# Kernel optimization log

Hardware: AMD Instinct MI355X
Metric: run time of the kernel (lower is better)

The kernel has to match this reference:

```python
import jax, jax.numpy as jnp
import numpy as np
import math

T, S, B, E, H = 2048, 2048, 4, 1024, 16
D = E // H


def setup_inputs() -> dict:
    key = jax.random.key(0)
    ks = jax.random.split(key, 12)
    inp = {
        "query": jax.random.normal(ks[0], (T, B, E), jnp.float32),
        "key": jax.random.normal(ks[1], (S, B, E), jnp.float32),
        "value": jax.random.normal(ks[2], (S, B, E), jnp.float32),
        # causal mask: True means masked (matches torch masked_fill semantics)
        "attn_mask": jnp.triu(jnp.ones((T, S), dtype=bool), k=1),
        # torch Linear layout: weight [out_features, in_features]
        "Wq": jax.random.normal(ks[3], (E, E), jnp.float32) * (1.0 / math.sqrt(E)),
        "bq": jax.random.normal(ks[4], (E,), jnp.float32) * 0.02,
        "Wk": jax.random.normal(ks[5], (E, E), jnp.float32) * (1.0 / math.sqrt(E)),
        "bk": jax.random.normal(ks[6], (E,), jnp.float32) * 0.02,
        "Wv": jax.random.normal(ks[7], (E, E), jnp.float32) * (1.0 / math.sqrt(E)),
        "bv": jax.random.normal(ks[8], (E,), jnp.float32) * 0.02,
        "Wo": jax.random.normal(ks[9], (E, E), jnp.float32) * (1.0 / math.sqrt(E)),
        "bo": jax.random.normal(ks[10], (E,), jnp.float32) * 0.02,
    }
    return inp


def reference(query, key, value, attn_mask, Wq, bq, Wk, bk, Wv, bv, Wo, bo):
    # inputs are [T/S, B, E] (batch_first=False); compute in [B, H, T, D]
    q = (jnp.einsum('tbe,fe->btf', query, Wq) + bq).reshape(B, T, H, D).transpose(0, 2, 1, 3)
    k = (jnp.einsum('sbe,fe->bsf', key, Wk) + bk).reshape(B, S, H, D).transpose(0, 2, 1, 3)
    v = (jnp.einsum('sbe,fe->bsf', value, Wv) + bv).reshape(B, S, H, D).transpose(0, 2, 1, 3)

    scores = jnp.einsum('bhtd,bhsd->bhts', q, k) / math.sqrt(D)  # [B,H,T,S]
    masked = jnp.where(attn_mask[None, None, :, :], -jnp.inf, scores)
    # custom numerics: epsilon-shifted softmax, then re-zero -inf positions
    probs = jax.nn.softmax(masked + 1e-9, axis=-1)
    probs = jnp.where(jnp.isinf(masked), 0.0, probs)

    out = jnp.einsum('bhts,bhsd->bhtd', probs, v)  # [B,H,T,D]
    out = out.transpose(0, 2, 1, 3).reshape(B, T, E)
    out = out @ Wo.T + bo
    return out.transpose(1, 0, 2)  # back to [T, B, E]
```

## Files before the change

### kernel.cpp

```cpp
#include <hip/hip_runtime.h>

typedef unsigned short u16;
typedef __attribute__((ext_vector_type(8))) __bf16 bf16x8;
typedef __attribute__((ext_vector_type(4))) float f32x4;
typedef __attribute__((ext_vector_type(16))) float f32x16;
typedef __attribute__((ext_vector_type(4))) unsigned short u16x4;
typedef __attribute__((ext_vector_type(8))) unsigned short u16x8;
typedef __attribute__((ext_vector_type(4))) unsigned int u32x4;

#define T_LEN 2048
#define B_SZ 4
#define E_DIM 1024
#define H_N 16
#define D_H 64
#define M_ROWS (T_LEN * B_SZ)
#define NQT (T_LEN / 128)

__device__ __forceinline__ u16 f2bf(float f){
  unsigned u = __builtin_bit_cast(unsigned, f);
  u += 0x7fffu + ((u >> 16) & 1u);
  return (u16)(u >> 16);
}

__device__ __forceinline__ float fexp2(float x){
#if __has_builtin(__builtin_amdgcn_exp2f)
  return __builtin_amdgcn_exp2f(x);
#else
  return exp2f(x);
#endif
}

__device__ __forceinline__ unsigned cvtpk(float lo, float hi){
  unsigned w;
  asm("v_cvt_pk_bf16_f32 %0, %1, %2" : "=v"(w) : "v"(lo), "v"(hi));
  return w;
}
__device__ __forceinline__ float xhalf_max(float x){
  return fmaxf(x, __shfl_xor(x, 32));
}
__device__ __forceinline__ float xhalf_sum(float x){
  return x + __shfl_xor(x, 32);
}

__device__ __forceinline__ void load_lds16(const void* g, void* l){
  __builtin_amdgcn_global_load_lds(
      (const __attribute__((address_space(1))) void*)g,
      (__attribute__((address_space(3))) void*)l, 16, 0, 0);
}

__global__ void cvt_all(
    const float* __restrict__ i0, const float* __restrict__ i1, const float* __restrict__ i2,
    const float* __restrict__ i3, const float* __restrict__ i4, const float* __restrict__ i5,
    const float* __restrict__ i6,
    u16* __restrict__ o0, u16* __restrict__ o1, u16* __restrict__ o2,
    u16* __restrict__ o3, u16* __restrict__ o4, u16* __restrict__ o5,
    u16* __restrict__ o6, int nX, int nW)
{
  const int z = blockIdx.z;
  const float* in; u16* out; int n;
  switch (z){
    case 0: in=i0; out=o0; n=nX; break;
    case 1: in=i1; out=o1; n=nX; break;
    case 2: in=i2; out=o2; n=nX; break;
    case 3: in=i3; out=o3; n=nW; break;
    case 4: in=i4; out=o4; n=nW; break;
    case 5: in=i5; out=o5; n=nW; break;
    default: in=i6; out=o6; n=nW; break;
  }
  int idx = (blockIdx.x * blockDim.x + threadIdx.x) * 4;
  int stride = gridDim.x * blockDim.x * 4;
  for (int i = idx; i < n; i += stride){
    float4 v = *(const float4*)(in + i);
    u16x4 o = { f2bf(v.x), f2bf(v.y), f2bf(v.z), f2bf(v.w) };
    *(u16x4*)(out + i) = o;
  }
}

__device__ __forceinline__ void gemm_mainloop(
    const u16* __restrict__ A, const u16* __restrict__ Bt,
    int m0, int n0, u16* As, u16* Bs, f32x4 (&acc)[4][4])
{
  constexpr int K = E_DIM;
  constexpr int NT = K / 32;
  const int tid = threadIdx.x;
  const int lane = tid & 63;
  const int w = tid >> 6;
  const int wr = w >> 1, wc = w & 1;
  const int lr = lane & 15, lg = lane >> 4;

  #pragma unroll
  for (int i=0;i<4;i++)
    #pragma unroll
    for (int j=0;j<4;j++) acc[i][j] = (f32x4){0.f,0.f,0.f,0.f};

  auto STAGE = [&](int t, int b){
    int k0 = t * 32;
    #pragma unroll
    for (int r=0;r<2;++r){
      int c = r*256 + tid;
      int row = c >> 2, cc = (c & 3) * 8;
      load_lds16(A  + (size_t)(m0 + row)*K + k0 + cc,
                 (char*)As + b*8192 + (r*256 + w*64)*16);
      load_lds16(Bt + (size_t)(n0 + row)*K + k0 + cc,
                 (char*)Bs + b*8192 + (r*256 + w*64)*16);
    }
  };

  STAGE(0, 0);
  __syncthreads();
  for (int t = 0; t < NT; ++t){
    const int cur = t & 1;
    if (t + 1 < NT) STAGE(t+1, cur^1);
    bf16x8 af[4], bfr[4];
    #pragma unroll
    for (int i=0;i<4;i++){
      af[i]  = *(const bf16x8*)&As[cur*4096 + (wr*64 + i*16 + lr)*32 + lg*8];
      bfr[i] = *(const bf16x8*)&Bs[cur*4096 + (wc*64 + i*16 + lr)*32 + lg*8];
    }
    #pragma unroll
    for (int i=0;i<4;i++)
      #pragma unroll
      for (int j=0;j<4;j++)
        acc[i][j] = __builtin_amdgcn_mfma_f32_16x16x32_bf16(af[i], bfr[j], acc[i][j], 0,0,0);
    __syncthreads();
  }
}

struct QKVArgs {
  const u16* A[3]; const u16* Bw[3]; const float* bias[3];
  float scale[3]; u16* out[3];
};

__global__ __launch_bounds__(256) void gemm_qkv(QKVArgs args){
  __shared__ __align__(16) u16 As[2*128*32];
  __shared__ __align__(16) u16 Bs[2*128*32];
  const int z = blockIdx.z;
  const int m0 = blockIdx.y * 128, n0 = blockIdx.x * 128;
  f32x4 acc[4][4];
  gemm_mainloop(args.A[z], args.Bw[z], m0, n0, As, Bs, acc);

  const int tid = threadIdx.x;
  const int lane = tid & 63;
  const int w = tid >> 6;
  const int wr = w >> 1, wc = w & 1;
  const int lr = lane & 15, lg = lane >> 4;
  const float* bias = args.bias[z];
  const float scale = args.scale[z];
  u16* outB = args.out[z];
  #pragma unroll
  for (int i=0;i<4;i++)
    #pragma unroll
    for (int j=0;j<4;j++)
      #pragma unroll
      for (int q=0;q<4;q++){
        int m = m0 + wr*64 + i*16 + lg*4 + q;
        int n = n0 + wc*64 + j*16 + lr;
        float v = (acc[i][j][q] + bias[n]) * scale;
        int t = m >> 2, b = m & 3;
        int h = n >> 6, d = n & 63;
        outB[ ((size_t)(b*H_N + h)*T_LEN + t)*D_H + d ] = f2bf(v);
      }
}

__global__ __launch_bounds__(256) void gemm_out(
    const u16* __restrict__ A, const u16* __restrict__ Bt,
    const float* __restrict__ bias, float* __restrict__ outF)
{
  __shared__ __align__(16) u16 As[2*128*32];
  __shared__ __align__(16) u16 Bs[2*128*32];
  const int m0 = blockIdx.y * 128, n0 = blockIdx.x * 128;
  f32x4 acc[4][4];
  gemm_mainloop(A, Bt, m0, n0, As, Bs, acc);

  const int tid = threadIdx.x;
  const int lane = tid & 63;
  const int w = tid >> 6;
  const int wr = w >> 1, wc = w & 1;
  const int lr = lane & 15, lg = lane >> 4;
  #pragma unroll
  for (int i=0;i<4;i++)
    #pragma unroll
    for (int j=0;j<4;j++)
      #pragma unroll
      for (int q=0;q<4;q++){
        int m = m0 + wr*64 + i*16 + lg*4 + q;
        int n = n0 + wc*64 + j*16 + lr;
        float v = acc[i][j][q] + bias[n];
        int b = m >> 11, t = m & 2047;
        outF[ (size_t)(t*B_SZ + b)*E_DIM + n ] = v;
      }
}

__global__ __launch_bounds__(256) void transpose_v(const u16* __restrict__ Vb, u16* __restrict__ Vt){
  __shared__ u16 tile[64][65];
  int bh = blockIdx.y, s0 = blockIdx.x * 64;
  const u16* src = Vb + ((size_t)bh*T_LEN + s0)*D_H;
  u16* dst = Vt + (size_t)bh*D_H*T_LEN + s0;
  int tid = threadIdx.x;
  #pragma unroll
  for (int r=0;r<2;++r){
    int c = r*256 + tid;
    int s = c >> 3, d0 = (c & 7)*8;
    u16x8 v = *(const u16x8*)(src + (size_t)s*D_H + d0);
    #pragma unroll
    for (int j=0;j<8;j++) tile[d0+j][s] = v[j];
  }
  __syncthreads();
  #pragma unroll
  for (int r=0;r<2;++r){
    int c = r*256 + tid;
    int d = c >> 3, s1 = (c & 7)*8;
    u16x8 v;
    #pragma unroll
    for (int j=0;j<8;j++){
      int p = s1 + j;
      int sp = (p & ~12) | ((p & 4) << 1) | ((p & 8) >> 1);
      v[j] = tile[d][sp];
    }
    *(u16x8*)(dst + (size_t)d*T_LEN + s1) = v;
  }
}

__global__ __launch_bounds__(256) void attn_fwd(
    const u16* __restrict__ Qb, const u16* __restrict__ Kb,
    const u16* __restrict__ Vt, u16* __restrict__ AO)
{
  __shared__ __align__(16) u16 smem[4*64*64];
  u16* Ks = smem;
  u16* Vs = smem + 2*64*64;
  const int tid = threadIdx.x;
  const int lane = tid & 63;
  const int wq = tid >> 6;
  const int l31 = lane & 31;
  const int hi = lane >> 5;
  const int bh = blockIdx.y;
  const u16* Kbase = Kb + (size_t)bh * T_LEN * D_H;
  const u16* Vbase = Vt + (size_t)bh * D_H * T_LEN;
  const int b_ = bh >> 4, h = bh & 15;

  auto STAGE = [&](int j, int b){
    int s0 = j * 64;
    #pragma unroll
    for (int r=0;r<2;++r){
      int c = r*256 + tid;
      int row = c >> 3;
      int colb = (c & 7) * 16;
      int scolb = colb ^ ((row & 7) << 4);
      load_lds16((const char*)(Kbase + (size_t)(s0 + row)*D_H) + scolb,
                 (char*)Ks + b*8192 + (r*256 + wq*64)*16);
      load_lds16((const char*)(Vbase + (size_t)row*T_LEN + s0) + scolb,
                 (char*)Vs + b*8192 + (r*256 + wq*64)*16);
    }
  };

  #pragma unroll 1
  for (int ph = 0; ph < 2; ++ph){
    const int qt = ph ? blockIdx.x : (NQT - 1 - blockIdx.x);
    const int qb = qt * 128;
    const int qg = qb + wq*32 + l31;

    bf16x8 qf[4];
    {
      const u16* qp = Qb + (size_t)bh*T_LEN*D_H + (size_t)qg*D_H + hi*8;
      #pragma unroll
      for (int kk=0;kk<4;++kk) qf[kk] = *(const bf16x8*)(qp + kk*16);
    }

    f32x16 o[2];
    #pragma unroll
    for (int f=0;f<2;++f)
      #pragma unroll
      for (int r=0;r<16;++r) o[f][r] = 0.f;
    float m_run = -INFINITY, l_run = 0.f;

    const int ntiles = 2*qt + 2;
    __syncthreads();
    STAGE(0, 0);
    __syncthreads();

    for (int j = 0; j < ntiles; ++j){
      const int cur = j & 1;
      if (j + 1 < ntiles) STAGE(j+1, cur^1);
      const char* Kc = (const char*)Ks + cur*8192;
      const char* Vc = (const char*)Vs + cur*8192;

      const bool fullmask = (j == 2*qt + 1) && (wq < 2);
      if (!fullmask){
        f32x16 st[2];
        #pragma unroll
        for (int i=0;i<2;++i)
          #pragma unroll
          for (int r=0;r<16;++r) st[i][r] = 0.f;
        __builtin_amdgcn_s_setprio(1);
        #pragma unroll
        for (int i=0;i<2;++i){
          #pragma unroll
          for (int kk=0;kk<4;++kk){
            int row = i*32 + l31;
            int colb = (kk*32 + hi*16) ^ ((row & 7) << 4);
            bf16x8 kf = *(const bf16x8*)(Kc + row*128 + colb);
            st[i] = __builtin_amdgcn_mfma_f32_32x32x16_bf16(kf, qf[kk], st[i], 0,0,0);
          }
        }
        __builtin_amdgcn_s_setprio(0);

        const int s0 = j*64;
        float mx = -INFINITY;
        if (j >= 2*qt){
          #pragma unroll
          for (int i=0;i<2;++i)
            #pragma unroll
            for (int r=0;r<16;++r){
              int sg = s0 + i*32 + (r&3) + 8*(r>>2) + 4*hi;
              float v = (sg > qg) ? -INFINITY : st[i][r];
              st[i][r] = v;
              mx = fmaxf(mx, v);
            }
        } else {
          #pragma unroll
          for (int i=0;i<2;++i)
            #pragma unroll
            for (int r=0;r<16;++r) mx = fmaxf(mx, st[i][r]);
        }
        mx = xhalf_max(mx);

        if (!__all(mx <= m_run + 8.0f)){
          float m_new = fmaxf(m_run, mx);
          float sc = fexp2(m_run - m_new);
          l_run *= sc;
          #pragma unroll
          for (int f=0;f<2;++f)
            #pragma unroll
            for (int r=0;r<16;++r) o[f][r] *= sc;
          m_run = m_new;
        }

        float rsum = 0.f;
        #pragma unroll
        for (int i=0;i<2;++i)
          #pragma unroll
          for (int r=0;r<16;++r){
            float p = fexp2(st[i][r] - m_run);
            st[i][r] = p;
            rsum += p;
          }
        l_run += xhalf_sum(rsum);

        u32x4 Bfr[4];
        #pragma unroll
        for (int i=0;i<2;++i){
          Bfr[2*i]   = (u32x4){ cvtpk(st[i][0],  st[i][1]),  cvtpk(st[i][2],  st[i][3]),
                                cvtpk(st[i][4],  st[i][5]),  cvtpk(st[i][6],  st[i][7]) };
          Bfr[2*i+1] = (u32x4){ cvtpk(st[i][8],  st[i][9]),  cvtpk(st[i][10], st[i][11]),
                                cvtpk(st[i][12], st[i][13]), cvtpk(st[i][14], st[i][15]) };
        }

        __builtin_amdgcn_s_setprio(1);
        #pragma unroll
        for (int ss=0; ss<4; ++ss){
          bf16x8 pb = __builtin_bit_cast(bf16x8, Bfr[ss]);
          #pragma unroll
          for (int f=0; f<2; ++f){
            int row = f*32 + l31;
            int colb = (ss*32 + hi*16) ^ ((row & 7) << 4);
            bf16x8 vf = *(const bf16x8*)(Vc + row*128 + colb);
            o[f] = __builtin_amdgcn_mfma_f32_32x32x16_bf16(vf, pb, o[f], 0,0,0);
          }
        }
        __builtin_amdgcn_s_setprio(0);
      }
      __syncthreads();
    }

    float linv = 1.f / l_run;
    {
      char* Osh = (char*)smem;
      unsigned base = wq*4352;
      #pragma unroll
      for (int f=0;f<2;++f)
        #pragma unroll
        for (int m=0;m<8;++m){
          unsigned word = cvtpk(o[f][2*m]*linv, o[f][2*m+1]*linv);
          int d0 = (m&1)*2 + 8*(m>>1) + 4*hi + 32*f;
          *(unsigned*)(Osh + base + l31*136 + d0*2) = word;
        }
    }
    __syncthreads();
    {
      int q = tid >> 1, half = tid & 1;
      const char* src = (const char*)smem + (q>>5)*4352 + (q&31)*136 + half*64;
      u16* dst = AO + ((size_t)(b_*T_LEN + qb + q))*E_DIM + h*D_H + half*32;
      #pragma unroll
      for (int k=0;k<4;++k)
        *(u16x8*)(dst + k*8) = *(const u16x8*)(src + k*16);
    }
  }
}

extern "C" void kernel_launch(void* const* d_in, const int* in_sizes, int n_in,
                              void* d_out, int out_size, void* d_ws, size_t ws_size,
                              hipStream_t stream){
  const float* query = (const float*)d_in[0];
  const float* key   = (const float*)d_in[1];
  const float* value = (const float*)d_in[2];
  const float* Wq = (const float*)d_in[4];
  const float* bq = (const float*)d_in[5];
  const float* Wk = (const float*)d_in[6];
  const float* bk = (const float*)d_in[7];
  const float* Wv = (const float*)d_in[8];
  const float* bv = (const float*)d_in[9];
  const float* Wo = (const float*)d_in[10];
  const float* bo = (const float*)d_in[11];

  char* ws = (char*)d_ws;
  const size_t SZ_X = (size_t)M_ROWS * E_DIM * 2;
  const size_t SZ_W = (size_t)E_DIM * E_DIM * 2;
  u16* Xq  = (u16*)(ws);
  u16* Xk  = (u16*)(ws + SZ_X);
  u16* Xv  = (u16*)(ws + 2*SZ_X);
  u16* Wqb = (u16*)(ws + 3*SZ_X);
  u16* Wkb = (u16*)(ws + 3*SZ_X + 1*SZ_W);
  u16* Wvb = (u16*)(ws + 3*SZ_X + 2*SZ_W);
  u16* Wob = (u16*)(ws + 3*SZ_X + 3*SZ_W);
  u16* Qb  = (u16*)(ws + 3*SZ_X + 4*SZ_W);
  u16* Kb  = (u16*)(ws + 4*SZ_X + 4*SZ_W);
  u16* Vb  = (u16*)(ws + 5*SZ_X + 4*SZ_W);
  u16* Vt  = Xk;
  u16* AO  = Xq;

  const int nX = M_ROWS * E_DIM;
  const int nW = E_DIM * E_DIM;
  cvt_all<<<dim3(1024,1,7), 256, 0, stream>>>(
      query, key, value, Wq, Wk, Wv, Wo,
      Xq, Xk, Xv, Wqb, Wkb, Wvb, Wob, nX, nW);

  const float QSCALE = 0.125f * 1.44269504f;
  QKVArgs qa;
  qa.A[0]=Xq;  qa.A[1]=Xk;  qa.A[2]=Xv;
  qa.Bw[0]=Wqb; qa.Bw[1]=Wkb; qa.Bw[2]=Wvb;
  qa.bias[0]=bq; qa.bias[1]=bk; qa.bias[2]=bv;
  qa.scale[0]=QSCALE; qa.scale[1]=1.0f; qa.scale[2]=1.0f;
  qa.out[0]=Qb; qa.out[1]=Kb; qa.out[2]=Vb;
  gemm_qkv<<<dim3(E_DIM/128, M_ROWS/128, 3), 256, 0, stream>>>(qa);
  transpose_v<<<dim3(T_LEN/64, B_SZ*H_N), 256, 0, stream>>>(Vb, Vt);
  attn_fwd<<<dim3(NQT/2, B_SZ*H_N), 256, 0, stream>>>(Qb, Kb, Vt, AO);
  gemm_out<<<dim3(E_DIM/128, M_ROWS/128), 256, 0, stream>>>(AO, Wob, bo, (float*)d_out);
}
```

Before: 210.8 us.

## Rewrite projection GEMMs with 256x128 tiles, triple-buffered swizzled LDS, XCD remap

Replaces the 128x128, K=32 double-buffered GEMM mainloop with a 512-thread 256x128 tile and K=64 steps. Global-to-LDS loads run through a three-stage ring in XOR-swizzled LDS, and the next stages' loads are interleaved with MFMA groups under explicit waitcnt and barriers plus raised priority. Both GEMMs and the attention kernel remap block indices so neighbouring tiles land on the same XCD for better L2 reuse. The aim is to cut LDS bank conflicts and exposed memory latency and to raise MFMA utilisation. The cost is one block per CU with about 144KB of LDS, and hand-tuned vmcnt counts that are fragile.

Result: faster. 184.7 us (-12.4%).

```diff
diff --git a/kernel.cpp b/kernel.cpp
--- a/kernel.cpp
+++ b/kernel.cpp
@@ -76,54 +76,121 @@
   }
 }
 
-__device__ __forceinline__ void gemm_mainloop(
+#define GEMM_LDSU16 73728
+
+__device__ __forceinline__ void stageA8(const u16* __restrict__ A, int m0, int k0, int r,
+                                        char* Ab, int tid){
+  int c = r*512 + tid;
+  int row = c >> 3;
+  int colb = ((c & 7) * 16) ^ ((row & 7) << 4);
+  load_lds16((const char*)(A + (size_t)(m0 + row)*E_DIM + k0) + colb,
+             Ab + (size_t)(r*512 + (tid >> 6)*64)*16);
+}
+__device__ __forceinline__ void stageB8(const u16* __restrict__ Bt, int n0, int k0, int r,
+                                        char* Bb, int tid){
+  int c = r*512 + tid;
+  int row = c >> 3;
+  int colb = ((c & 7) * 16) ^ ((row & 7) << 4);
+  load_lds16((const char*)(Bt + (size_t)(n0 + row)*E_DIM + k0) + colb,
+             Bb + (size_t)(r*512 + (tid >> 6)*64)*16);
+}
+
+__device__ __forceinline__ void gemm8_mainloop(
     const u16* __restrict__ A, const u16* __restrict__ Bt,
-    int m0, int n0, u16* As, u16* Bs, f32x4 (&acc)[4][4])
+    int m0, int n0, u16* smem, f32x4 (&acc)[8][2])
 {
-  constexpr int K = E_DIM;
-  constexpr int NT = K / 32;
+  constexpr int NT = E_DIM / 64;
   const int tid = threadIdx.x;
   const int lane = tid & 63;
   const int w = tid >> 6;
-  const int wr = w >> 1, wc = w & 1;
+  const int wm = w >> 2, wn = w & 3;
   const int lr = lane & 15, lg = lane >> 4;
-
-  #pragma unroll
-  for (int i=0;i<4;i++)
-    #pragma unroll
-    for (int j=0;j<4;j++) acc[i][j] = (f32x4){0.f,0.f,0.f,0.f};
-
-  auto STAGE = [&](int t, int b){
-    int k0 = t * 32;
-    #pragma unroll
-    for (int r=0;r<2;++r){
-      int c = r*256 + tid;
-      int row = c >> 2, cc = (c & 3) * 8;
-      load_lds16(A  + (size_t)(m0 + row)*K + k0 + cc,
-                 (char*)As + b*8192 + (r*256 + w*64)*16);
-      load_lds16(Bt + (size_t)(n0 + row)*K + k0 + cc,
-                 (char*)Bs + b*8192 + (r*256 + w*64)*16);
-    }
-  };
-
-  STAGE(0, 0);
-  __syncthreads();
+  char* Abase = (char*)smem;
+  char* Bbase = (char*)smem + 98304;
+
+  #pragma unroll
+  for (int i=0;i<8;i++)
+    #pragma unroll
+    for (int j=0;j<2;j++) acc[i][j] = (f32x4){0.f,0.f,0.f,0.f};
+
+  #pragma unroll
+  for (int r=0;r<4;++r) stageA8(A, m0, 0, r, Abase, tid);
+  #pragma unroll
+  for (int r=0;r<2;++r) stageB8(Bt, n0, 0, r, Bbase, tid);
+  #pragma unroll
+  for (int r=0;r<4;++r) stageA8(A, m0, 64, r, Abase + 32768, tid);
+  #pragma unroll
+  for (int r=0;r<2;++r) stageB8(Bt, n0, 64, r, Bbase + 16384, tid);
+  asm volatile("s_waitcnt vmcnt(6)\n" ::: "memory");
+  __builtin_amdgcn_sched_barrier(0);
+  __builtin_amdgcn_s_barrier();
+
+  int buf = 0;
+  const int cb0 = (lr & 7) << 4;
   for (int t = 0; t < NT; ++t){
-    const int cur = t & 1;
-    if (t + 1 < NT) STAGE(t+1, cur^1);
-    bf16x8 af[4], bfr[4];
-    #pragma unroll
-    for (int i=0;i<4;i++){
-      af[i]  = *(const bf16x8*)&As[cur*4096 + (wr*64 + i*16 + lr)*32 + lg*8];
-      bfr[i] = *(const bf16x8*)&Bs[cur*4096 + (wc*64 + i*16 + lr)*32 + lg*8];
-    }
-    #pragma unroll
-    for (int i=0;i<4;i++)
-      #pragma unroll
-      for (int j=0;j<4;j++)
-        acc[i][j] = __builtin_amdgcn_mfma_f32_16x16x32_bf16(af[i], bfr[j], acc[i][j], 0,0,0);
-    __syncthreads();
-  }
+    char* Ac = Abase + buf*32768;
+    char* Bc = Bbase + buf*16384;
+    int nbuf = buf + 1; if (nbuf == 3) nbuf = 0;
+    int sbuf = nbuf + 1; if (sbuf == 3) sbuf = 0;
+    char* As = Abase + sbuf*32768;
+    char* Bs = Bbase + sbuf*16384;
+    const int k2 = (t + 2) * 64;
+    const bool has2 = (t + 2 < NT);
+    bf16x8 bfrag[2][2];
+
+    #pragma unroll
+    for (int p = 0; p < 4; ++p){
+      const int r0 = wm*128 + (2*p)*16 + lr;
+      const int r1 = r0 + 16;
+      bf16x8 a00 = *(const bf16x8*)(Ac + r0*128 + ((lg*16)      ^ cb0));
+      bf16x8 a01 = *(const bf16x8*)(Ac + r0*128 + ((lg*16 + 64) ^ cb0));
+      bf16x8 a10 = *(const bf16x8*)(Ac + r1*128 + ((lg*16)      ^ cb0));
+      bf16x8 a11 = *(const bf16x8*)(Ac + r1*128 + ((lg*16 + 64) ^ cb0));
+      if (p == 0){
+        #pragma unroll
+        for (int j=0;j<2;++j){
+          int rb = wn*32 + j*16 + lr;
+          bfrag[j][0] = *(const bf16x8*)(Bc + rb*128 + ((lg*16)      ^ cb0));
+          bfrag[j][1] = *(const bf16x8*)(Bc + rb*128 + ((lg*16 + 64) ^ cb0));
+        }
+      }
+      if (has2){
+        if (p == 0){ stageA8(A, m0, k2, 0, As, tid); stageA8(A, m0, k2, 1, As, tid); }
+        else if (p == 1){ stageA8(A, m0, k2, 2, As, tid); stageA8(A, m0, k2, 3, As, tid); }
+        else if (p == 2){ stageB8(Bt, n0, k2, 0, Bs, tid); stageB8(Bt, n0, k2, 1, Bs, tid); }
+      }
+      __builtin_amdgcn_s_barrier();
+      asm volatile("s_waitcnt lgkmcnt(0)\n" ::: "memory");
+      __builtin_amdgcn_sched_barrier(0);
+      __builtin_amdgcn_s_setprio(1);
+      const int i0 = 2*p, i1 = 2*p + 1;
+      acc[i0][0] = __builtin_amdgcn_mfma_f32_16x16x32_bf16(a00, bfrag[0][0], acc[i0][0], 0,0,0);
+      acc[i0][0] = __builtin_amdgcn_mfma_f32_16x16x32_bf16(a01, bfrag[0][1], acc[i0][0], 0,0,0);
+      acc[i0][1] = __builtin_amdgcn_mfma_f32_16x16x32_bf16(a00, bfrag[1][0], acc[i0][1], 0,0,0);
+      acc[i0][1] = __builtin_amdgcn_mfma_f32_16x16x32_bf16(a01, bfrag[1][1], acc[i0][1], 0,0,0);
+      acc[i1][0] = __builtin_amdgcn_mfma_f32_16x16x32_bf16(a10, bfrag[0][0], acc[i1][0], 0,0,0);
+      acc[i1][0] = __builtin_amdgcn_mfma_f32_16x16x32_bf16(a11, bfrag[0][1], acc[i1][0], 0,0,0);
+      acc[i1][1] = __builtin_amdgcn_mfma_f32_16x16x32_bf16(a10, bfrag[1][0], acc[i1][1], 0,0,0);
+      acc[i1][1] = __builtin_amdgcn_mfma_f32_16x16x32_bf16(a11, bfrag[1][1], acc[i1][1], 0,0,0);
+      __builtin_amdgcn_s_setprio(0);
+      if (p == 3){
+        if (t < NT-2)       asm volatile("s_waitcnt vmcnt(6)\n" ::: "memory");
+        else if (t == NT-2) asm volatile("s_waitcnt vmcnt(0)\n" ::: "memory");
+        __builtin_amdgcn_sched_barrier(0);
+      }
+      __builtin_amdgcn_s_barrier();
+    }
+    buf = nbuf;
+  }
+  __builtin_amdgcn_sched_barrier(0);
+}
+
+__device__ __forceinline__ void xcd_remap_gemm(int &m0, int &n0){
+  int L = blockIdx.y * 8 + blockIdx.x;
+  int c = L & 7, i = L >> 3;
+  int by = c*4 + (i & 3);
+  int bx = i >> 2;
+  m0 = by * 256; n0 = bx * 128;
 }
 
 struct QKVArgs {
@@ -131,30 +198,28 @@
   float scale[3]; u16* out[3];
 };
 
-__global__ __launch_bounds__(256) void gemm_qkv(QKVArgs args){
-  __shared__ __align__(16) u16 As[2*128*32];
-  __shared__ __align__(16) u16 Bs[2*128*32];
+__global__ __launch_bounds__(512, 1) void gemm_qkv(QKVArgs args){
+  __shared__ __align__(16) u16 smem[GEMM_LDSU16];
   const int z = blockIdx.z;
-  const int m0 = blockIdx.y * 128, n0 = blockIdx.x * 128;
-  f32x4 acc[4][4];
-  gemm_mainloop(args.A[z], args.Bw[z], m0, n0, As, Bs, acc);
-
-  const int tid = threadIdx.x;
-  const int lane = tid & 63;
-  const int w = tid >> 6;
-  const int wr = w >> 1, wc = w & 1;
+  int m0, n0; xcd_remap_gemm(m0, n0);
+  f32x4 acc[8][2];
+  gemm8_mainloop(args.A[z], args.Bw[z], m0, n0, smem, acc);
+
+  const int lane = threadIdx.x & 63;
+  const int w = threadIdx.x >> 6;
+  const int wm = w >> 2, wn = w & 3;
   const int lr = lane & 15, lg = lane >> 4;
   const float* bias = args.bias[z];
   const float scale = args.scale[z];
   u16* outB = args.out[z];
   #pragma unroll
-  for (int i=0;i<4;i++)
-    #pragma unroll
-    for (int j=0;j<4;j++)
+  for (int i=0;i<8;i++)
+    #pragma unroll
+    for (int j=0;j<2;j++)
       #pragma unroll
       for (int q=0;q<4;q++){
-        int m = m0 + wr*64 + i*16 + lg*4 + q;
-        int n = n0 + wc*64 + j*16 + lr;
+        int m = m0 + wm*128 + i*16 + lg*4 + q;
+        int n = n0 + wn*32 + j*16 + lr;
         float v = (acc[i][j][q] + bias[n]) * scale;
         int t = m >> 2, b = m & 3;
         int h = n >> 6, d = n & 63;
@@ -162,29 +227,27 @@
       }
 }
 
-__global__ __launch_bounds__(256) void gemm_out(
+__global__ __launch_bounds__(512, 1) void gemm_out(
     const u16* __restrict__ A, const u16* __restrict__ Bt,
     const float* __restrict__ bias, float* __restrict__ outF)
 {
-  __shared__ __align__(16) u16 As[2*128*32];
-  __shared__ __align__(16) u16 Bs[2*128*32];
-  const int m0 = blockIdx.y * 128, n0 = blockIdx.x * 128;
-  f32x4 acc[4][4];
-  gemm_mainloop(A, Bt, m0, n0, As, Bs, acc);
-
-  const int tid = threadIdx.x;
-  const int lane = tid & 63;
-  const int w = tid >> 6;
-  const int wr = w >> 1, wc = w & 1;
+  __shared__ __align__(16) u16 smem[GEMM_LDSU16];
+  int m0, n0; xcd_remap_gemm(m0, n0);
+  f32x4 acc[8][2];
+  gemm8_mainloop(A, Bt, m0, n0, smem, acc);
+
+  const int lane = threadIdx.x & 63;
+  const int w = threadIdx.x >> 6;
+  const int wm = w >> 2, wn = w & 3;
   const int lr = lane & 15, lg = lane >> 4;
   #pragma unroll
-  for (int i=0;i<4;i++)
-    #pragma unroll
-    for (int j=0;j<4;j++)
+  for (int i=0;i<8;i++)
+    #pragma unroll
+    for (int j=0;j<2;j++)
       #pragma unroll
       for (int q=0;q<4;q++){
-        int m = m0 + wr*64 + i*16 + lg*4 + q;
-        int n = n0 + wc*64 + j*16 + lr;
+        int m = m0 + wm*128 + i*16 + lg*4 + q;
+        int n = n0 + wn*32 + j*16 + lr;
         float v = acc[i][j][q] + bias[n];
         int b = m >> 11, t = m & 2047;
         outF[ (size_t)(t*B_SZ + b)*E_DIM + n ] = v;
@@ -233,7 +296,13 @@
   const int wq = tid >> 6;
   const int l31 = lane & 31;
   const int hi = lane >> 5;
-  const int bh = blockIdx.y;
+  int bh, px;
+  {
+    int L = blockIdx.y * 8 + blockIdx.x;
+    int c = L & 7, i2 = L >> 3;
+    bh = c*8 + (i2 & 7);
+    px = i2 >> 3;
+  }
   const u16* Kbase = Kb + (size_t)bh * T_LEN * D_H;
   const u16* Vbase = Vt + (size_t)bh * D_H * T_LEN;
   const int b_ = bh >> 4, h = bh & 15;
@@ -255,7 +324,7 @@
 
   #pragma unroll 1
   for (int ph = 0; ph < 2; ++ph){
-    const int qt = ph ? blockIdx.x : (NQT - 1 - blockIdx.x);
+    const int qt = ph ? px : (NQT - 1 - px);
     const int qb = qt * 128;
     const int qg = qb + wq*32 + l31;
 
@@ -441,8 +510,8 @@
   qa.bias[0]=bq; qa.bias[1]=bk; qa.bias[2]=bv;
   qa.scale[0]=QSCALE; qa.scale[1]=1.0f; qa.scale[2]=1.0f;
   qa.out[0]=Qb; qa.out[1]=Kb; qa.out[2]=Vb;
-  gemm_qkv<<<dim3(E_DIM/128, M_ROWS/128, 3), 256, 0, stream>>>(qa);
+  gemm_qkv<<<dim3(8, M_ROWS/256, 3), 512, 0, stream>>>(qa);
   transpose_v<<<dim3(T_LEN/64, B_SZ*H_N), 256, 0, stream>>>(Vb, Vt);
   attn_fwd<<<dim3(NQT/2, B_SZ*H_N), 256, 0, stream>>>(Qb, Kb, Vt, AO);
-  gemm_out<<<dim3(E_DIM/128, M_ROWS/128), 256, 0, stream>>>(AO, Wob, bo, (float*)d_out);
-}
+  gemm_out<<<dim3(8, M_ROWS/256), 512, 0, stream>>>(AO, Wob, bo, (float*)d_out);
+}
```

## Use 4-stage LDS pipeline with swizzle and XCD-aware block remap in GEMMs

Applied to the files above, without the earlier changes.

The GEMM mainloop moves from double buffering to a 4-buffer ring with prefetch distance 2. It uses explicit vmcnt/lgkmcnt waits and raw s_barrier in place of __syncthreads, and raises wave priority around the MFMA burst. LDS columns are XOR-swizzled to cut bank conflicts, and block indices in both GEMMs and the attention kernel are remapped so neighbouring tiles land on the same XCD for L2 reuse. The cost is doubled LDS per block (64KB), which may lower occupancy, and hand-written wait counts that must match the exact number of outstanding loads.

Result: faster. 180.7 us (-14.3%).

```diff
diff --git a/kernel.cpp b/kernel.cpp
--- a/kernel.cpp
+++ b/kernel.cpp
@@ -76,54 +76,84 @@
   }
 }
 
-__device__ __forceinline__ void gemm_mainloop(
+#define G4_LDSU16 32768
+
+__device__ __forceinline__ void stageG(const u16* __restrict__ G, int r0g, int k0,
+                                       char* base, int buf, int tid){
+  #pragma unroll
+  for (int r=0;r<2;++r){
+    int c = r*256 + tid;
+    int row = c >> 2;
+    int colb = ((c & 3) * 16) ^ (((row >> 2) & 3) << 4);
+    load_lds16((const char*)(G + (size_t)(r0g + row)*E_DIM + k0) + colb,
+               base + buf*8192 + (size_t)(r*256 + (tid >> 6)*64)*16);
+  }
+}
+
+__device__ __forceinline__ void gemm4_mainloop(
     const u16* __restrict__ A, const u16* __restrict__ Bt,
-    int m0, int n0, u16* As, u16* Bs, f32x4 (&acc)[4][4])
+    int m0, int n0, u16* smem, f32x4 (&acc)[4][4])
 {
-  constexpr int K = E_DIM;
-  constexpr int NT = K / 32;
+  constexpr int NT = E_DIM / 32;
   const int tid = threadIdx.x;
   const int lane = tid & 63;
   const int w = tid >> 6;
   const int wr = w >> 1, wc = w & 1;
   const int lr = lane & 15, lg = lane >> 4;
+  char* Abase = (char*)smem;
+  char* Bbase = (char*)smem + 32768;
 
   #pragma unroll
   for (int i=0;i<4;i++)
     #pragma unroll
     for (int j=0;j<4;j++) acc[i][j] = (f32x4){0.f,0.f,0.f,0.f};
 
-  auto STAGE = [&](int t, int b){
-    int k0 = t * 32;
-    #pragma unroll
-    for (int r=0;r<2;++r){
-      int c = r*256 + tid;
-      int row = c >> 2, cc = (c & 3) * 8;
-      load_lds16(A  + (size_t)(m0 + row)*K + k0 + cc,
-                 (char*)As + b*8192 + (r*256 + w*64)*16);
-      load_lds16(Bt + (size_t)(n0 + row)*K + k0 + cc,
-                 (char*)Bs + b*8192 + (r*256 + w*64)*16);
-    }
-  };
-
-  STAGE(0, 0);
-  __syncthreads();
+  stageG(A,  m0, 0,  Abase, 0, tid);
+  stageG(Bt, n0, 0,  Bbase, 0, tid);
+  stageG(A,  m0, 32, Abase, 1, tid);
+  stageG(Bt, n0, 32, Bbase, 1, tid);
+  asm volatile("s_waitcnt vmcnt(4)\n" ::: "memory");
+  __builtin_amdgcn_sched_barrier(0);
+  __builtin_amdgcn_s_barrier();
+
+  const int cbx = (lg*16) ^ (((lr >> 2) & 3) << 4);
+
   for (int t = 0; t < NT; ++t){
-    const int cur = t & 1;
-    if (t + 1 < NT) STAGE(t+1, cur^1);
+    const int buf = t & 3;
+    if (t + 2 < NT){
+      stageG(A,  m0, (t+2)*32, Abase, (t+2) & 3, tid);
+      stageG(Bt, n0, (t+2)*32, Bbase, (t+2) & 3, tid);
+    }
+    char* Ac = Abase + buf*8192;
+    char* Bc = Bbase + buf*8192;
     bf16x8 af[4], bfr[4];
     #pragma unroll
     for (int i=0;i<4;i++){
-      af[i]  = *(const bf16x8*)&As[cur*4096 + (wr*64 + i*16 + lr)*32 + lg*8];
-      bfr[i] = *(const bf16x8*)&Bs[cur*4096 + (wc*64 + i*16 + lr)*32 + lg*8];
-    }
+      af[i]  = *(const bf16x8*)(Ac + (wr*64 + i*16 + lr)*64 + cbx);
+      bfr[i] = *(const bf16x8*)(Bc + (wc*64 + i*16 + lr)*64 + cbx);
+    }
+    asm volatile("s_waitcnt lgkmcnt(0)\n" ::: "memory");
+    __builtin_amdgcn_sched_barrier(0);
+    __builtin_amdgcn_s_setprio(1);
     #pragma unroll
     for (int i=0;i<4;i++)
       #pragma unroll
       for (int j=0;j<4;j++)
         acc[i][j] = __builtin_amdgcn_mfma_f32_16x16x32_bf16(af[i], bfr[j], acc[i][j], 0,0,0);
-    __syncthreads();
-  }
+    __builtin_amdgcn_s_setprio(0);
+    if (t + 2 < NT)      asm volatile("s_waitcnt vmcnt(4)\n" ::: "memory");
+    else if (t + 1 < NT) asm volatile("s_waitcnt vmcnt(0)\n" ::: "memory");
+    __builtin_amdgcn_sched_barrier(0);
+    __builtin_amdgcn_s_barrier();
+  }
+}
+
+__device__ __forceinline__ void xcd_remap_gemm(int &m0, int &n0){
+  int L = blockIdx.y * 8 + blockIdx.x;
+  int c = L & 7, i = L >> 3;
+  int by = c*8 + (i & 7);
+  int bx = i >> 3;
+  m0 = by * 128; n0 = bx * 128;
 }
 
 struct QKVArgs {
@@ -132,16 +162,14 @@
 };
 
 __global__ __launch_bounds__(256) void gemm_qkv(QKVArgs args){
-  __shared__ __align__(16) u16 As[2*128*32];
-  __shared__ __align__(16) u16 Bs[2*128*32];
+  __shared__ __align__(16) u16 smem[G4_LDSU16];
   const int z = blockIdx.z;
-  const int m0 = blockIdx.y * 128, n0 = blockIdx.x * 128;
+  int m0, n0; xcd_remap_gemm(m0, n0);
   f32x4 acc[4][4];
-  gemm_mainloop(args.A[z], args.Bw[z], m0, n0, As, Bs, acc);
-
-  const int tid = threadIdx.x;
-  const int lane = tid & 63;
-  const int w = tid >> 6;
+  gemm4_mainloop(args.A[z], args.Bw[z], m0, n0, smem, acc);
+
+  const int lane = threadIdx.x & 63;
+  const int w = threadIdx.x >> 6;
   const int wr = w >> 1, wc = w & 1;
   const int lr = lane & 15, lg = lane >> 4;
   const float* bias = args.bias[z];
@@ -166,15 +194,13 @@
     const u16* __restrict__ A, const u16* __restrict__ Bt,
     const float* __restrict__ bias, float* __restrict__ outF)
 {
-  __shared__ __align__(16) u16 As[2*128*32];
-  __shared__ __align__(16) u16 Bs[2*128*32];
-  const int m0 = blockIdx.y * 128, n0 = blockIdx.x * 128;
+  __shared__ __align__(16) u16 smem[G4_LDSU16];
+  int m0, n0; xcd_remap_gemm(m0, n0);
   f32x4 acc[4][4];
-  gemm_mainloop(A, Bt, m0, n0, As, Bs, acc);
-
-  const int tid = threadIdx.x;
-  const int lane = tid & 63;
-  const int w = tid >> 6;
+  gemm4_mainloop(A, Bt, m0, n0, smem, acc);
+
+  const int lane = threadIdx.x & 63;
+  const int w = threadIdx.x >> 6;
   const int wr = w >> 1, wc = w & 1;
   const int lr = lane & 15, lg = lane >> 4;
   #pragma unroll
@@ -233,7 +259,13 @@
   const int wq = tid >> 6;
   const int l31 = lane & 31;
   const int hi = lane >> 5;
-  const int bh = blockIdx.y;
+  int bh, px;
+  {
+    int L = blockIdx.y * 8 + blockIdx.x;
+    int c = L & 7, i2 = L >> 3;
+    bh = c*8 + (i2 & 7);
+    px = i2 >> 3;
+  }
   const u16* Kbase = Kb + (size_t)bh * T_LEN * D_H;
   const u16* Vbase = Vt + (size_t)bh * D_H * T_LEN;
   const int b_ = bh >> 4, h = bh & 15;
@@ -255,7 +287,7 @@
 
   #pragma unroll 1
   for (int ph = 0; ph < 2; ++ph){
-    const int qt = ph ? blockIdx.x : (NQT - 1 - blockIdx.x);
+    const int qt = ph ? px : (NQT - 1 - px);
     const int qb = qt * 128;
     const int qg = qb + wq*32 + l31;
 
@@ -441,8 +473,8 @@
   qa.bias[0]=bq; qa.bias[1]=bk; qa.bias[2]=bv;
   qa.scale[0]=QSCALE; qa.scale[1]=1.0f; qa.scale[2]=1.0f;
   qa.out[0]=Qb; qa.out[1]=Kb; qa.out[2]=Vb;
-  gemm_qkv<<<dim3(E_DIM/128, M_ROWS/128, 3), 256, 0, stream>>>(qa);
+  gemm_qkv<<<dim3(8, M_ROWS/128, 3), 256, 0, stream>>>(qa);
   transpose_v<<<dim3(T_LEN/64, B_SZ*H_N), 256, 0, stream>>>(Vb, Vt);
   attn_fwd<<<dim3(NQT/2, B_SZ*H_N), 256, 0, stream>>>(Qb, Kb, Vt, AO);
-  gemm_out<<<dim3(E_DIM/128, M_ROWS/128), 256, 0, stream>>>(AO, Wob, bo, (float*)d_out);
-}
+  gemm_out<<<dim3(8, M_ROWS/128), 256, 0, stream>>>(AO, Wob, bo, (float*)d_out);
+}
```
